# Kernel optimization log

Measured on AMD Instinct MI355X. Metric: run time of the kernel, lower is better.

Reference implementation:

```python
import jax, jax.numpy as jnp
import numpy as np

ALPHA = 0.2   # LeakyReLU negative slope
NEG = -1e9    # mask value for non-edges


def setup_inputs() -> dict:
    key = jax.random.key(0)
    ks = jax.random.split(key, 8)
    N, Din, F, H, Dout = 4096, 512, 64, 8, 16
    adj = (jax.random.uniform(ks[0], (N, N)) < 0.01).astype(jnp.float32)
    adjacency = jnp.maximum(adj, jnp.eye(N, dtype=jnp.float32))
    X = jax.random.normal(ks[1], (N, Din), jnp.float32)
    s = lambda k, shape, fan: jax.random.normal(k, shape, jnp.float32) / np.float32(np.sqrt(fan))
    W = s(ks[2], (H, Din, F), Din)        # per-head projection, stacked
    a1 = s(ks[3], (H, F), F)              # attention vector, source half
    a2 = s(ks[4], (H, F), F)              # attention vector, target half
    Wo = s(ks[5], (H * F, Dout), H * F)   # output-layer projection
    ao1 = s(ks[6], (Dout,), Dout)
    ao2 = s(ks[7], (Dout,), Dout)
    return dict(adjacency=adjacency, X=X, W=W, a1=a1, a2=a2, Wo=Wo, ao1=ao1, ao2=ao2)


def reference(adjacency, X, W, a1, a2, Wo, ao1, ao2):
    # dropout is identity (eval mode / p=0)
    mask = adjacency > 0
    N = X.shape[0]
    # --- multi-head attention layers (concat=True -> ELU) ---
    Wh = jnp.einsum('nd,hdf->hnf', X, W)                      # [H, N, F]
    f1 = jnp.einsum('hnf,hf->hn', Wh, a1)                     # [H, N]
    f2 = jnp.einsum('hnf,hf->hn', Wh, a2)                     # [H, N]
    e = jax.nn.leaky_relu(f1[:, :, None] + f2[:, None, :], ALPHA)  # [H, N, N]
    att = jax.nn.softmax(jnp.where(mask[None], e, NEG), axis=-1)
    heads = jax.nn.elu(jnp.einsum('hnm,hmf->hnf', att, Wh))   # [H, N, F]
    cat = jnp.transpose(heads, (1, 0, 2)).reshape(N, -1)      # [N, H*F]
    # --- output attention layer (concat=False -> no ELU) ---
    Who = cat @ Wo                                            # [N, Dout]
    eo = jax.nn.leaky_relu((Who @ ao1)[:, None] + (Who @ ao2)[None, :], ALPHA)
    atto = jax.nn.softmax(jnp.where(mask, eo, NEG), axis=-1)  # [N, N]
    return atto @ Who                                         # [N, Dout]
```

## Files before the change

kernel.cpp:

```cpp
#include <hip/hip_runtime.h>
#include <hip/hip_bf16.h>

#define N_NODES 4096
#define DIN     512
#define FDIM    64
#define NHEADS  8
#define DOUT    16
#define MAXN    512

typedef __attribute__((ext_vector_type(8))) short bf16x8;
typedef __attribute__((ext_vector_type(4))) float f32x4;

static __device__ __forceinline__ float us2f(unsigned short u) {
    union { unsigned int i; float f; } cv; cv.i = ((unsigned int)u) << 16; return cv.f;
}
static __device__ __forceinline__ unsigned short f2us(float v) {
    __hip_bfloat16 b = __float2bfloat16(v);
    return *(const unsigned short*)&b;
}
static __device__ __forceinline__ int is_f32(const void* adj) {
    return (((const unsigned short*)adj)[0] == 0) ? 1 : 0;
}

__global__ __launch_bounds__(256) void prep_kernel(
    const void* __restrict__ adj, const void* __restrict__ X, const void* __restrict__ W,
    const void* __restrict__ a1, const void* __restrict__ a2, const void* __restrict__ Wo,
    const void* __restrict__ ao1, const void* __restrict__ ao2,
    unsigned short* __restrict__ Xb, unsigned short* __restrict__ Wt,
    float* __restrict__ Woc,
    float* __restrict__ a1c, float* __restrict__ a2c,
    float* __restrict__ ao1c, float* __restrict__ ao2c)
{
    const int f32 = is_f32(adj);
    const int i0 = blockIdx.x * 256 + threadIdx.x;
    const int T = 1024 * 256;
    for (int i = i0; i < N_NODES * DIN; i += T) {
        float v = f32 ? ((const float*)X)[i] : us2f(((const unsigned short*)X)[i]);
        Xb[i] = f2us(v);
    }
    for (int i = i0; i < NHEADS * DIN * FDIM; i += T) {
        int hh = i >> 15, rem = i & 32767, d = rem >> 6, f = rem & 63;
        float v = f32 ? ((const float*)W)[i] : us2f(((const unsigned short*)W)[i]);
        Wt[((size_t)(hh * FDIM + f)) * DIN + d] = f2us(v);
    }
    if (i0 < DIN * DOUT) {
        float v = f32 ? ((const float*)Wo)[i0] : us2f(((const unsigned short*)Wo)[i0]);
        Woc[i0] = v;
    }
    if (i0 < 512) {
        a1c[i0] = f32 ? ((const float*)a1)[i0] : us2f(((const unsigned short*)a1)[i0]);
        a2c[i0] = f32 ? ((const float*)a2)[i0] : us2f(((const unsigned short*)a2)[i0]);
    }
    if (i0 < 16) {
        ao1c[i0] = f32 ? ((const float*)ao1)[i0] : us2f(((const unsigned short*)ao1)[i0]);
        ao2c[i0] = f32 ? ((const float*)ao2)[i0] : us2f(((const unsigned short*)ao2)[i0]);
    }
}

__global__ __launch_bounds__(256) void wh_f12_kernel(
    const unsigned short* __restrict__ Xb, const unsigned short* __restrict__ Wt,
    const float* __restrict__ a1c, const float* __restrict__ a2c,
    unsigned short* __restrict__ Whb, float* __restrict__ f1, float* __restrict__ f2)
{
    const int h  = blockIdx.x;
    const int bm = blockIdx.y;
    const int w    = threadIdx.x >> 6;
    const int lane = threadIdx.x & 63;
    const int quad = lane >> 4;
    const int l16  = lane & 15;
    const int node = bm * 64 + w * 16 + l16;

    f32x4 acc[4];
#pragma unroll
    for (int j = 0; j < 4; ++j) acc[j] = (f32x4){0.f, 0.f, 0.f, 0.f};

    const unsigned short* xp = Xb + (size_t)node * DIN + quad * 8;
    const unsigned short* wp = Wt + (size_t)h * FDIM * DIN + quad * 8;
#pragma unroll 4
    for (int k0 = 0; k0 < DIN; k0 += 32) {
        bf16x8 b = *(const bf16x8*)(xp + k0);
#pragma unroll
        for (int j = 0; j < 4; ++j) {
            bf16x8 a = *(const bf16x8*)(wp + (size_t)(j * 16 + l16) * DIN + k0);
            acc[j] = __builtin_amdgcn_mfma_f32_16x16x32_bf16(a, b, acc[j], 0, 0, 0);
        }
    }
    float p1 = 0.f, p2 = 0.f;
#pragma unroll
    for (int j = 0; j < 4; ++j) {
        const int fbase = j * 16 + quad * 4;
        ushort4 st;
        st.x = f2us(acc[j][0]); st.y = f2us(acc[j][1]);
        st.z = f2us(acc[j][2]); st.w = f2us(acc[j][3]);
        *(ushort4*)&Whb[((size_t)node * NHEADS + h) * FDIM + fbase] = st;
#pragma unroll
        for (int rr = 0; rr < 4; ++rr) {
            p1 += acc[j][rr] * a1c[h * FDIM + fbase + rr];
            p2 += acc[j][rr] * a2c[h * FDIM + fbase + rr];
        }
    }
    p1 += __shfl_xor(p1, 16); p1 += __shfl_xor(p1, 32);
    p2 += __shfl_xor(p2, 16); p2 += __shfl_xor(p2, 32);
    if (quad == 0) {
        f1[h * N_NODES + node] = p1;
        f2[h * N_NODES + node] = p2;
    }
}

__global__ __launch_bounds__(256) void attn1_fused_kernel(
    const void* __restrict__ adj,
    const unsigned short* __restrict__ Whb,
    const float* __restrict__ f1, const float* __restrict__ f2,
    const float* __restrict__ Woc,
    const float* __restrict__ ao1c, const float* __restrict__ ao2c,
    int* __restrict__ cnt, int* __restrict__ nbr,
    float* __restrict__ Who, float* __restrict__ g1, float* __restrict__ g2)
{
    const int n   = blockIdx.x;
    const int tid = threadIdx.x;
    const int wv  = tid >> 6;
    const int lane = tid & 63;

    __shared__ int   sh_m[MAXN];
    __shared__ int   sh_c;
    __shared__ float sh_s[NHEADS][516];
    __shared__ float sh_inv[NHEADS];
    __shared__ float sh_red[3][64][9];
    __shared__ float cat_sh[512];
    __shared__ float sh_p[16 * 17];

    if (tid == 0) sh_c = 0;
    __syncthreads();
    if (is_f32(adj)) {
        const uint4* row = (const uint4*)((const unsigned int*)adj + (size_t)n * N_NODES);
#pragma unroll 4
        for (int q = tid; q < N_NODES / 4; q += 256) {
            uint4 v = row[q];
            int base = q * 4;
            if (v.x) { int p = atomicAdd(&sh_c, 1); if (p < MAXN) sh_m[p] = base + 0; }
            if (v.y) { int p = atomicAdd(&sh_c, 1); if (p < MAXN) sh_m[p] = base + 1; }
            if (v.z) { int p = atomicAdd(&sh_c, 1); if (p < MAXN) sh_m[p] = base + 2; }
            if (v.w) { int p = atomicAdd(&sh_c, 1); if (p < MAXN) sh_m[p] = base + 3; }
        }
    } else {
        const ushort4* row = (const ushort4*)((const unsigned short*)adj + (size_t)n * N_NODES);
#pragma unroll 4
        for (int q = tid; q < N_NODES / 4; q += 256) {
            ushort4 v = row[q];
            int base = q * 4;
            if (v.x) { int p = atomicAdd(&sh_c, 1); if (p < MAXN) sh_m[p] = base + 0; }
            if (v.y) { int p = atomicAdd(&sh_c, 1); if (p < MAXN) sh_m[p] = base + 1; }
            if (v.z) { int p = atomicAdd(&sh_c, 1); if (p < MAXN) sh_m[p] = base + 2; }
            if (v.w) { int p = atomicAdd(&sh_c, 1); if (p < MAXN) sh_m[p] = base + 3; }
        }
    }
    __syncthreads();
    const int c = (sh_c < MAXN) ? sh_c : MAXN;
    for (int k = tid; k < c; k += 256) nbr[(size_t)n * MAXN + k] = sh_m[k];
    if (tid == 0) cnt[n] = c;

    const int h = tid >> 5;
    const int l32 = tid & 31;
    const float f1v = f1[h * N_NODES + n];
    float mx = -1e30f;
    for (int k = l32; k < c; k += 32) {
        float s = f1v + f2[h * N_NODES + sh_m[k]];
        s = (s >= 0.f) ? s : 0.2f * s;
        sh_s[h][k] = s;
        mx = fmaxf(mx, s);
    }
#pragma unroll
    for (int off = 16; off; off >>= 1) mx = fmaxf(mx, __shfl_xor(mx, off));
    float sum = 0.f;
    for (int k = l32; k < c; k += 32) {
        float e = __expf(sh_s[h][k] - mx);
        sh_s[h][k] = e;
        sum += e;
    }
#pragma unroll
    for (int off = 16; off; off >>= 1) sum += __shfl_xor(sum, off);
    if (l32 == 0) sh_inv[h] = (sum > 0.f) ? 1.f / sum : 0.f;
    __syncthreads();

    const int hh = lane >> 3;
    float acc8[8];
#pragma unroll
    for (int e = 0; e < 8; ++e) acc8[e] = 0.f;
    const uint4* wb = (const uint4*)Whb;
#pragma unroll 2
    for (int kb = 0; kb < c; kb += 4) {
        const int k = kb + wv;
        float wgt = 0.f; int m = sh_m[0];
        if (k < c) { wgt = sh_s[hh][k]; m = sh_m[k]; }
        uint4 v = wb[(size_t)m * 64 + lane];
        acc8[0] += wgt * us2f((unsigned short)(v.x & 0xFFFFu));
        acc8[1] += wgt * us2f((unsigned short)(v.x >> 16));
        acc8[2] += wgt * us2f((unsigned short)(v.y & 0xFFFFu));
        acc8[3] += wgt * us2f((unsigned short)(v.y >> 16));
        acc8[4] += wgt * us2f((unsigned short)(v.z & 0xFFFFu));
        acc8[5] += wgt * us2f((unsigned short)(v.z >> 16));
        acc8[6] += wgt * us2f((unsigned short)(v.w & 0xFFFFu));
        acc8[7] += wgt * us2f((unsigned short)(v.w >> 16));
    }
    if (wv) {
#pragma unroll
        for (int e = 0; e < 8; ++e) sh_red[wv - 1][lane][e] = acc8[e];
    }
    __syncthreads();
    if (wv == 0) {
        const float inv = sh_inv[hh];
#pragma unroll
        for (int e = 0; e < 8; ++e) {
            float s = acc8[e] + sh_red[0][lane][e] + sh_red[1][lane][e] + sh_red[2][lane][e];
            s *= inv;
            s = (s > 0.f) ? s : expm1f(s);
            cat_sh[lane * 8 + e] = s;
        }
    }
    __syncthreads();

    {
        const int j = tid & 15, ch = tid >> 4;
        float s = 0.f;
#pragma unroll
        for (int d = 0; d < 32; ++d)
            s += cat_sh[ch * 32 + d] * Woc[(ch * 32 + d) * DOUT + j];
        sh_p[ch * 17 + j] = s;
    }
    __syncthreads();
    if (tid < 16) {
        float s = 0.f;
#pragma unroll
        for (int ch = 0; ch < 16; ++ch) s += sh_p[ch * 17 + tid];
        Who[n * DOUT + tid] = s;
        float p1 = s * ao1c[tid];
        float p2 = s * ao2c[tid];
#pragma unroll
        for (int off = 8; off; off >>= 1) {
            p1 += __shfl_xor(p1, off);
            p2 += __shfl_xor(p2, off);
        }
        if (tid == 0) { g1[n] = p1; g2[n] = p2; }
    }
}

__global__ __launch_bounds__(64) void attn2_kernel(
    const void* __restrict__ adj,
    const float* __restrict__ Who,
    const float* __restrict__ g1, const float* __restrict__ g2,
    const int* __restrict__ cnt, const int* __restrict__ nbr,
    void* __restrict__ out)
{
    const int n = blockIdx.x;
    const int lane = threadIdx.x;
    const int quad = lane >> 4, l16 = lane & 15;
    __shared__ float sh_s[MAXN];
    __shared__ int sh_m[MAXN];
    const int c0 = cnt[n];
    const int c = (c0 < MAXN) ? c0 : MAXN;
    for (int k = lane; k < c; k += 64) sh_m[k] = nbr[(size_t)n * MAXN + k];
    __syncthreads();
    const float gn = g1[n];
    float mx = -1e30f;
    for (int k = lane; k < c; k += 64) {
        float s = gn + g2[sh_m[k]];
        s = (s >= 0.f) ? s : 0.2f * s;
        sh_s[k] = s;
        mx = fmaxf(mx, s);
    }
#pragma unroll
    for (int off = 32; off; off >>= 1) mx = fmaxf(mx, __shfl_xor(mx, off));
    __syncthreads();
    float sum = 0.f;
    for (int k = lane; k < c; k += 64) {
        float e = __expf(sh_s[k] - mx);
        sh_s[k] = e;
        sum += e;
    }
#pragma unroll
    for (int off = 32; off; off >>= 1) sum += __shfl_xor(sum, off);
    __syncthreads();
    const float inv = (sum > 0.f) ? 1.f / sum : 0.f;
    float accv = 0.f;
#pragma unroll 4
    for (int k = quad; k < c; k += 4)
        accv += sh_s[k] * Who[sh_m[k] * DOUT + l16];
    accv += __shfl_xor(accv, 16);
    accv += __shfl_xor(accv, 32);
    if (quad == 0) {
        float v = accv * inv;
        if (is_f32(adj)) ((float*)out)[n * DOUT + l16] = v;
        else             ((unsigned short*)out)[n * DOUT + l16] = f2us(v);
    }
}

__global__ void wsfail_kernel(float* __restrict__ out)
{
    if (threadIdx.x == 0) out[0] = 129.f;
}

extern "C" void kernel_launch(void* const* d_in, const int* in_sizes, int n_in,
                              void* d_out, int out_size, void* d_ws, size_t ws_size,
                              hipStream_t stream)
{
    const void* adj = d_in[0];
    const void* X   = d_in[1];
    const void* W   = d_in[2];
    const void* a1  = d_in[3];
    const void* a2  = d_in[4];
    const void* Wo  = d_in[5];
    const void* ao1 = d_in[6];
    const void* ao2 = d_in[7];

    const size_t NEEDED = 22000000;
    if (ws_size < NEEDED) { wsfail_kernel<<<1, 64, 0, stream>>>((float*)d_out); return; }

    int*   cnt  = (int*)d_ws;
    int*   nbr  = cnt + 4096;
    float* a1c  = (float*)(nbr + 2097152);
    float* a2c  = a1c + 512;
    float* ao1c = a2c + 512;
    float* ao2c = ao1c + 16;
    float* f1   = ao2c + 16;
    float* f2   = f1 + 32768;
    float* Who  = f2 + 32768;
    float* g1   = Who + 65536;
    float* g2   = g1 + 4096;
    float* Woc  = g2 + 4096;
    unsigned short* Whb = (unsigned short*)(Woc + 8192);
    unsigned short* Xb  = Whb + 2097152;
    unsigned short* Wt  = Xb + 2097152;

    prep_kernel<<<1024, 256, 0, stream>>>(
        adj, X, W, a1, a2, Wo, ao1, ao2,
        Xb, Wt, Woc, a1c, a2c, ao1c, ao2c);
    wh_f12_kernel<<<dim3(NHEADS, N_NODES / 64), 256, 0, stream>>>(
        Xb, Wt, a1c, a2c, Whb, f1, f2);
    attn1_fused_kernel<<<N_NODES, 256, 0, stream>>>(
        adj, Whb, f1, f2, Woc, ao1c, ao2c, cnt, nbr, Who, g1, g2);
    attn2_kernel<<<N_NODES, 64, 0, stream>>>(adj, Who, g1, g2, cnt, nbr, d_out);
}
```

Before: 174.2 us.

## Move neighbor extraction into prep kernel and use online softmax in attention

Adjacency row scanning and neighbor-list building move out of the first attention kernel into extra blocks of the prep kernel, which writes cnt/nbr straight to global memory. The attention kernel then loads the neighbor list and computes the softmax online in a single pass. Each of the four waves keeps its own running max and sum, with lazy rescaling, and the partials are merged at the end. This removes the separate score and max/exp passes through shared memory and lets the adjacency scan overlap with the dtype-conversion work. In exchange the neighbor list takes a global round trip, the nbr writes are scattered, and the per-edge gather loop now also does an exp and a branch.

Measured after the change: 163.3 us. -6.2%, faster.

```diff
diff --git a/kernel.cpp b/kernel.cpp
--- a/kernel.cpp
+++ b/kernel.cpp
@@ -22,16 +22,47 @@
     return (((const unsigned short*)adj)[0] == 0) ? 1 : 0;
 }
 
-__global__ __launch_bounds__(256) void prep_kernel(
+__global__ __launch_bounds__(256) void prep_nbr_kernel(
     const void* __restrict__ adj, const void* __restrict__ X, const void* __restrict__ W,
     const void* __restrict__ a1, const void* __restrict__ a2, const void* __restrict__ Wo,
     const void* __restrict__ ao1, const void* __restrict__ ao2,
     unsigned short* __restrict__ Xb, unsigned short* __restrict__ Wt,
     float* __restrict__ Woc,
     float* __restrict__ a1c, float* __restrict__ a2c,
-    float* __restrict__ ao1c, float* __restrict__ ao2c)
+    float* __restrict__ ao1c, float* __restrict__ ao2c,
+    int* __restrict__ cnt, int* __restrict__ nbr)
 {
     const int f32 = is_f32(adj);
+    if (blockIdx.x >= 1024) {
+        const int n = blockIdx.x - 1024;
+        __shared__ int c;
+        if (threadIdx.x == 0) c = 0;
+        __syncthreads();
+        if (f32) {
+            const uint4* row = (const uint4*)((const unsigned int*)adj + (size_t)n * N_NODES);
+            for (int q = threadIdx.x; q < N_NODES / 4; q += 256) {
+                uint4 v = row[q];
+                int base = q * 4;
+                if (v.x) { int p = atomicAdd(&c, 1); if (p < MAXN) nbr[(size_t)n * MAXN + p] = base + 0; }
+                if (v.y) { int p = atomicAdd(&c, 1); if (p < MAXN) nbr[(size_t)n * MAXN + p] = base + 1; }
+                if (v.z) { int p = atomicAdd(&c, 1); if (p < MAXN) nbr[(size_t)n * MAXN + p] = base + 2; }
+                if (v.w) { int p = atomicAdd(&c, 1); if (p < MAXN) nbr[(size_t)n * MAXN + p] = base + 3; }
+            }
+        } else {
+            const ushort4* row = (const ushort4*)((const unsigned short*)adj + (size_t)n * N_NODES);
+            for (int q = threadIdx.x; q < N_NODES / 4; q += 256) {
+                ushort4 v = row[q];
+                int base = q * 4;
+                if (v.x) { int p = atomicAdd(&c, 1); if (p < MAXN) nbr[(size_t)n * MAXN + p] = base + 0; }
+                if (v.y) { int p = atomicAdd(&c, 1); if (p < MAXN) nbr[(size_t)n * MAXN + p] = base + 1; }
+                if (v.z) { int p = atomicAdd(&c, 1); if (p < MAXN) nbr[(size_t)n * MAXN + p] = base + 2; }
+                if (v.w) { int p = atomicAdd(&c, 1); if (p < MAXN) nbr[(size_t)n * MAXN + p] = base + 3; }
+            }
+        }
+        __syncthreads();
+        if (threadIdx.x == 0) cnt[n] = (c < MAXN) ? c : MAXN;
+        return;
+    }
     const int i0 = blockIdx.x * 256 + threadIdx.x;
     const int T = 1024 * 256;
     for (int i = i0; i < N_NODES * DIN; i += T) {
@@ -107,82 +138,33 @@
     }
 }
 
-__global__ __launch_bounds__(256) void attn1_fused_kernel(
-    const void* __restrict__ adj,
+__global__ __launch_bounds__(256) void attn1_kernel(
     const unsigned short* __restrict__ Whb,
     const float* __restrict__ f1, const float* __restrict__ f2,
     const float* __restrict__ Woc,
     const float* __restrict__ ao1c, const float* __restrict__ ao2c,
-    int* __restrict__ cnt, int* __restrict__ nbr,
+    const int* __restrict__ cnt, const int* __restrict__ nbr,
     float* __restrict__ Who, float* __restrict__ g1, float* __restrict__ g2)
 {
     const int n   = blockIdx.x;
     const int tid = threadIdx.x;
     const int wv  = tid >> 6;
     const int lane = tid & 63;
+    const int hh = lane >> 3;
 
     __shared__ int   sh_m[MAXN];
-    __shared__ int   sh_c;
-    __shared__ float sh_s[NHEADS][516];
-    __shared__ float sh_inv[NHEADS];
     __shared__ float sh_red[3][64][9];
+    __shared__ float sh_ml[4][NHEADS][2];
     __shared__ float cat_sh[512];
     __shared__ float sh_p[16 * 17];
 
-    if (tid == 0) sh_c = 0;
-    __syncthreads();
-    if (is_f32(adj)) {
-        const uint4* row = (const uint4*)((const unsigned int*)adj + (size_t)n * N_NODES);
-#pragma unroll 4
-        for (int q = tid; q < N_NODES / 4; q += 256) {
-            uint4 v = row[q];
-            int base = q * 4;
-            if (v.x) { int p = atomicAdd(&sh_c, 1); if (p < MAXN) sh_m[p] = base + 0; }
-            if (v.y) { int p = atomicAdd(&sh_c, 1); if (p < MAXN) sh_m[p] = base + 1; }
-            if (v.z) { int p = atomicAdd(&sh_c, 1); if (p < MAXN) sh_m[p] = base + 2; }
-            if (v.w) { int p = atomicAdd(&sh_c, 1); if (p < MAXN) sh_m[p] = base + 3; }
-        }
-    } else {
-        const ushort4* row = (const ushort4*)((const unsigned short*)adj + (size_t)n * N_NODES);
-#pragma unroll 4
-        for (int q = tid; q < N_NODES / 4; q += 256) {
-            ushort4 v = row[q];
-            int base = q * 4;
-            if (v.x) { int p = atomicAdd(&sh_c, 1); if (p < MAXN) sh_m[p] = base + 0; }
-            if (v.y) { int p = atomicAdd(&sh_c, 1); if (p < MAXN) sh_m[p] = base + 1; }
-            if (v.z) { int p = atomicAdd(&sh_c, 1); if (p < MAXN) sh_m[p] = base + 2; }
-            if (v.w) { int p = atomicAdd(&sh_c, 1); if (p < MAXN) sh_m[p] = base + 3; }
-        }
-    }
-    __syncthreads();
-    const int c = (sh_c < MAXN) ? sh_c : MAXN;
-    for (int k = tid; k < c; k += 256) nbr[(size_t)n * MAXN + k] = sh_m[k];
-    if (tid == 0) cnt[n] = c;
-
-    const int h = tid >> 5;
-    const int l32 = tid & 31;
-    const float f1v = f1[h * N_NODES + n];
-    float mx = -1e30f;
-    for (int k = l32; k < c; k += 32) {
-        float s = f1v + f2[h * N_NODES + sh_m[k]];
-        s = (s >= 0.f) ? s : 0.2f * s;
-        sh_s[h][k] = s;
-        mx = fmaxf(mx, s);
-    }
-#pragma unroll
-    for (int off = 16; off; off >>= 1) mx = fmaxf(mx, __shfl_xor(mx, off));
-    float sum = 0.f;
-    for (int k = l32; k < c; k += 32) {
-        float e = __expf(sh_s[h][k] - mx);
-        sh_s[h][k] = e;
-        sum += e;
-    }
-#pragma unroll
-    for (int off = 16; off; off >>= 1) sum += __shfl_xor(sum, off);
-    if (l32 == 0) sh_inv[h] = (sum > 0.f) ? 1.f / sum : 0.f;
-    __syncthreads();
-
-    const int hh = lane >> 3;
+    const int c0 = cnt[n];
+    const int c = (c0 < MAXN) ? c0 : MAXN;
+    for (int k = tid; k < c; k += 256) sh_m[k] = nbr[(size_t)n * MAXN + k];
+    __syncthreads();
+
+    const float f1v = f1[hh * N_NODES + n];
+    float m_run = -1e30f, l_run = 0.f;
     float acc8[8];
 #pragma unroll
     for (int e = 0; e < 8; ++e) acc8[e] = 0.f;
@@ -190,28 +172,51 @@
 #pragma unroll 2
     for (int kb = 0; kb < c; kb += 4) {
         const int k = kb + wv;
-        float wgt = 0.f; int m = sh_m[0];
-        if (k < c) { wgt = sh_s[hh][k]; m = sh_m[k]; }
-        uint4 v = wb[(size_t)m * 64 + lane];
-        acc8[0] += wgt * us2f((unsigned short)(v.x & 0xFFFFu));
-        acc8[1] += wgt * us2f((unsigned short)(v.x >> 16));
-        acc8[2] += wgt * us2f((unsigned short)(v.y & 0xFFFFu));
-        acc8[3] += wgt * us2f((unsigned short)(v.y >> 16));
-        acc8[4] += wgt * us2f((unsigned short)(v.z & 0xFFFFu));
-        acc8[5] += wgt * us2f((unsigned short)(v.z >> 16));
-        acc8[6] += wgt * us2f((unsigned short)(v.w & 0xFFFFu));
-        acc8[7] += wgt * us2f((unsigned short)(v.w >> 16));
+        if (k < c) {
+            const int mm = sh_m[k];
+            uint4 v = wb[(size_t)mm * 64 + lane];
+            float s = f1v + f2[hh * N_NODES + mm];
+            s = (s >= 0.f) ? s : 0.2f * s;
+            if (s > m_run + 8.f) {
+                float scale = __expf(m_run - s);
+                l_run *= scale;
+#pragma unroll
+                for (int e = 0; e < 8; ++e) acc8[e] *= scale;
+                m_run = s;
+            }
+            float wgt = __expf(s - m_run);
+            l_run += wgt;
+            acc8[0] += wgt * us2f((unsigned short)(v.x & 0xFFFFu));
+            acc8[1] += wgt * us2f((unsigned short)(v.x >> 16));
+            acc8[2] += wgt * us2f((unsigned short)(v.y & 0xFFFFu));
+            acc8[3] += wgt * us2f((unsigned short)(v.y >> 16));
+            acc8[4] += wgt * us2f((unsigned short)(v.z & 0xFFFFu));
+            acc8[5] += wgt * us2f((unsigned short)(v.z >> 16));
+            acc8[6] += wgt * us2f((unsigned short)(v.w & 0xFFFFu));
+            acc8[7] += wgt * us2f((unsigned short)(v.w >> 16));
+        }
     }
     if (wv) {
 #pragma unroll
         for (int e = 0; e < 8; ++e) sh_red[wv - 1][lane][e] = acc8[e];
     }
+    if ((lane & 7) == 0) {
+        sh_ml[wv][hh][0] = m_run;
+        sh_ml[wv][hh][1] = l_run;
+    }
     __syncthreads();
     if (wv == 0) {
-        const float inv = sh_inv[hh];
+        float m1 = sh_ml[1][hh][0], m2 = sh_ml[2][hh][0], m3 = sh_ml[3][hh][0];
+        float M = fmaxf(fmaxf(m_run, m1), fmaxf(m2, m3));
+        float c0f = __expf(m_run - M), c1f = __expf(m1 - M);
+        float c2f = __expf(m2 - M),  c3f = __expf(m3 - M);
+        float denom = l_run * c0f + sh_ml[1][hh][1] * c1f
+                    + sh_ml[2][hh][1] * c2f + sh_ml[3][hh][1] * c3f;
+        const float inv = (denom > 0.f) ? 1.f / denom : 0.f;
 #pragma unroll
         for (int e = 0; e < 8; ++e) {
-            float s = acc8[e] + sh_red[0][lane][e] + sh_red[1][lane][e] + sh_red[2][lane][e];
+            float s = acc8[e] * c0f + sh_red[0][lane][e] * c1f
+                    + sh_red[1][lane][e] * c2f + sh_red[2][lane][e] * c3f;
             s *= inv;
             s = (s > 0.f) ? s : expm1f(s);
             cat_sh[lane * 8 + e] = s;
@@ -331,12 +336,12 @@
     unsigned short* Xb  = Whb + 2097152;
     unsigned short* Wt  = Xb + 2097152;
 
-    prep_kernel<<<1024, 256, 0, stream>>>(
+    prep_nbr_kernel<<<1024 + N_NODES, 256, 0, stream>>>(
         adj, X, W, a1, a2, Wo, ao1, ao2,
-        Xb, Wt, Woc, a1c, a2c, ao1c, ao2c);
+        Xb, Wt, Woc, a1c, a2c, ao1c, ao2c, cnt, nbr);
     wh_f12_kernel<<<dim3(NHEADS, N_NODES / 64), 256, 0, stream>>>(
         Xb, Wt, a1c, a2c, Whb, f1, f2);
-    attn1_fused_kernel<<<N_NODES, 256, 0, stream>>>(
-        adj, Whb, f1, f2, Woc, ao1c, ao2c, cnt, nbr, Who, g1, g2);
+    attn1_kernel<<<N_NODES, 256, 0, stream>>>(
+        Whb, f1, f2, Woc, ao1c, ao2c, cnt, nbr, Who, g1, g2);
     attn2_kernel<<<N_NODES, 64, 0, stream>>>(adj, Who, g1, g2, cnt, nbr, d_out);
 }
```
